# Kernel tuning notes

Hardware: AMD Instinct MI355X
Metric: run time of the kernel (lower is better)

## Reference

```python
import jax, jax.numpy as jnp
import numpy as np

BS, SL, FD = 8192, 49, 11
D_MODEL, DM2, HEAD = 128, 64, 8
NH, NHID, NLAYER = DM2 // HEAD, 4, 2
ABF = 1.0
XY_IDX = np.array([0, 1, 2, 3, 4, 5, 6, 7, 10])  # x feats + y feat (batch-normed cols)
DEC_IN = D_MODEL + 10  # d_model + len(x_dims + spa_dims)


def tanhshrink(x):
    return x - jnp.tanh(x)


def rope_angles(spa):
    # spa: [bs, sl, 2] -> per-token block angles [bs, sl, 4]
    # block order matches torch.block_diag(Rx(t0), Ry(t0), Rx(t1), Ry(t1))
    thetas = 10000.0 ** ((2.0 - 2.0 * jnp.arange(2, dtype=spa.dtype)) / 8.0)  # d=8, n_thetas=2
    ax = spa[..., 0:1] * thetas  # [bs, sl, 2]
    ay = spa[..., 1:2] * thetas
    return jnp.stack([ax[..., 0], ay[..., 0], ax[..., 1], ay[..., 1]], axis=-1)


def apply_rope(v, ang):
    # v: [bs, nh, s, 8]; ang: [bs, s, 4]. Applies the 8x8 block-diagonal
    # rotation directly on 2-d sub-pairs (same math as R @ v, no 8x8 matmats).
    c = jnp.cos(ang)[:, None]  # [bs, 1, s, 4]
    s = jnp.sin(ang)[:, None]
    v2 = v.reshape(*v.shape[:-1], 4, 2)
    r = jnp.stack([c * v2[..., 0] - s * v2[..., 1],
                   s * v2[..., 0] + c * v2[..., 1]], axis=-1)
    return r.reshape(v.shape)


def heads(x):  # [bs, s, dm2] -> [bs, nh, s, hd]
    b, s, _ = x.shape
    return x.reshape(b, s, NH, HEAD).transpose(0, 2, 1, 3)


def merge(x):  # [bs, nh, s, hd] -> [bs, s, dm2]
    b, h, s, d = x.shape
    return x.transpose(0, 2, 1, 3).reshape(b, s, h * d)


def mlp2(x, w1, b1, w2, b2):
    return tanhshrink(x @ w1 + b1) @ w2 + b2


def forward_impl(input_tensor, dists, bn_gamma, bn_beta,
                 xe_w1, xe_b1, xe_w2, xe_b2, ye_w1, ye_b1, ye_w2, ye_b2,
                 learnable_y, hidden_tokens, Wq, Wk, Wv, Wo, Wq2, Wk2, Wv2, Wo2,
                 dec_w0, dec_b0, dec_w1, dec_b1, dec_w2, dec_b2):
    bs = input_tensor.shape[0]
    # --- NanBatchNorm over x+y feature columns (no NaNs in clean inputs) ---
    xy = input_tensor[:, :, XY_IDX]
    mu = jnp.mean(xy, axis=(0, 1), keepdims=True)
    var = jnp.var(xy, axis=(0, 1), keepdims=True)
    xy = (xy - mu) / jnp.sqrt(var + 1e-5) * bn_gamma + bn_beta
    input_tensor = input_tensor.at[:, :, XY_IDX].set(xy)

    # --- target at last seq position: drop its dist, keep context dists ---
    dists_ctx = dists[:, :-1]                       # [bs, sl-1]
    central_x = input_tensor[:, -1:, :-1]           # [bs, 1, 10] (x + spa feats)

    # --- 2D RoPE angles from spatial coords ---
    ang = rope_angles(input_tensor[:, :, 8:10])     # [bs, sl, 4]

    # --- FCN encoders (two streams a=x, b=y) ---
    x_embed = mlp2(input_tensor[:, :, :8], xe_w1, xe_b1, xe_w2, xe_b2)      # [bs, sl, 64]
    y_embed = mlp2(input_tensor[:, :-1, 10:11], ye_w1, ye_b1, ye_w2, ye_b2)  # [bs, sl-1, 64]
    y_embed = jnp.concatenate([y_embed, jnp.broadcast_to(learnable_y, (bs, 1, DM2))], axis=1)

    ctx = (x_embed[:, :-1], y_embed[:, :-1])
    qry = (x_embed[:, -1:], y_embed[:, -1:])
    ang_ctx, ang_q = ang[:, :-1], ang[:, -1:]
    bias = (-ABF * dists_ctx)[:, None, None, :]     # [bs, 1, 1, sl-1]
    scale = 1.0 / jnp.sqrt(jnp.asarray(HEAD, input_tensor.dtype))

    outs, attn_ws = [], []
    for s in range(2):
        H = jnp.broadcast_to(hidden_tokens, (bs, NHID, DM2))
        for l in range(NLAYER):
            q = heads(H @ Wq[l, s])
            k = apply_rope(heads(ctx[s] @ Wk[l, s]), ang_ctx)
            v = heads(ctx[s] @ Wv[l, s])
            sc = jnp.einsum('bhqd,bhkd->bhqk', q, k) * scale + bias
            a = jax.nn.softmax(sc, axis=-1)
            H = H + merge(jnp.einsum('bhqk,bhkd->bhqd', a, v)) @ Wo[l, s]
        # query cross-attends the inducing tokens
        q = apply_rope(heads(qry[s] @ Wq2[s]), ang_q)
        k = heads(H @ Wk2[s])
        v = heads(H @ Wv2[s])
        sc = jnp.einsum('bhqd,bhkd->bhqk', q, k) * scale
        a = jax.nn.softmax(sc, axis=-1)
        outs.append(merge(jnp.einsum('bhqk,bhkd->bhqd', a, v)) @ Wo2[s])  # [bs, 1, 64]
        attn_ws.append(a)

    encoding = jnp.concatenate(outs, axis=-1)               # [bs, 1, 128]
    encoding = jnp.concatenate([encoding, central_x], axis=-1)  # [bs, 1, 138]
    h = tanhshrink(encoding @ dec_w0 + dec_b0)
    h = tanhshrink(h @ dec_w1 + dec_b1)
    pred = h @ dec_w2 + dec_b2                              # [bs, 1, 1]
    return pred


def setup_inputs() -> dict:
    key = jax.random.key(0)
    ks = jax.random.split(key, 32)
    g = lambda i, shape: 0.05 * jax.random.normal(ks[i], shape, dtype=jnp.float32)
    inp = {
        'input_tensor': jax.random.normal(ks[0], (BS, SL, FD), dtype=jnp.float32),
        'dists': jax.random.uniform(ks[1], (BS, SL), dtype=jnp.float32),
        'target_position': jnp.zeros((3, BS), dtype=jnp.int32),
        'bn_gamma': jnp.ones((9,), jnp.float32),
        'bn_beta': jnp.zeros((9,), jnp.float32),
        'xe_w1': g(2, (8, DM2)), 'xe_b1': jnp.zeros((DM2,), jnp.float32),
        'xe_w2': g(3, (DM2, DM2)), 'xe_b2': jnp.zeros((DM2,), jnp.float32),
        'ye_w1': g(4, (1, DM2)), 'ye_b1': jnp.zeros((DM2,), jnp.float32),
        'ye_w2': g(5, (DM2, DM2)), 'ye_b2': jnp.zeros((DM2,), jnp.float32),
        'learnable_y': g(6, (1, 1, DM2)),
        'hidden_tokens': g(7, (NHID, DM2)),
        'Wq': g(8, (NLAYER, 2, DM2, DM2)), 'Wk': g(9, (NLAYER, 2, DM2, DM2)),
        'Wv': g(10, (NLAYER, 2, DM2, DM2)), 'Wo': g(11, (NLAYER, 2, DM2, DM2)),
        'Wq2': g(12, (2, DM2, DM2)), 'Wk2': g(13, (2, DM2, DM2)),
        'Wv2': g(14, (2, DM2, DM2)), 'Wo2': g(15, (2, DM2, DM2)),
        'dec_w0': g(16, (DEC_IN, 512)), 'dec_b0': jnp.zeros((512,), jnp.float32),
        'dec_w1': g(17, (512, 256)), 'dec_b1': jnp.zeros((256,), jnp.float32),
        'dec_w2': g(18, (256, 1)), 'dec_b2': jnp.zeros((1,), jnp.float32),
    }
    return inp


def reference(input_tensor, dists, target_position, bn_gamma, bn_beta,
              xe_w1, xe_b1, xe_w2, xe_b2, ye_w1, ye_b1, ye_w2, ye_b2,
              learnable_y, hidden_tokens, Wq, Wk, Wv, Wo, Wq2, Wk2, Wv2, Wo2,
              dec_w0, dec_b0, dec_w1, dec_b1, dec_w2, dec_b2):
    # target_position is an index constant (query is the last token by construction)
    return forward_impl(input_tensor, dists, bn_gamma, bn_beta,
                        xe_w1, xe_b1, xe_w2, xe_b2, ye_w1, ye_b1, ye_w2, ye_b2,
                        learnable_y, hidden_tokens, Wq, Wk, Wv, Wo, Wq2, Wk2, Wv2, Wo2,
                        dec_w0, dec_b0, dec_w1, dec_b1, dec_w2, dec_b2)
```

## Files before the change

### kernel.cpp

```cpp
#include <hip/hip_runtime.h>
#include <math.h>

#define BS 8192
#define SL 49
#define FDIM 11
#define ROWS (BS*SL)

__device__ __forceinline__ float tanhshrink_f(float x) {
  float e = __expf(2.f * x);
  return (x - 1.f) + __fdividef(2.f, e + 1.f);
}

__global__ __launch_bounds__(256) void k_stats(const float* __restrict__ inp,
                                               double* __restrict__ gsum) {
  const int nblk = gridDim.x;
  const int per = (ROWS + nblk - 1) / nblk;
  const int r0 = blockIdx.x * per;
  int r1 = r0 + per; if (r1 > ROWS) r1 = ROWS;
  float s[9], q[9];
#pragma unroll
  for (int j = 0; j < 9; ++j) { s[j] = 0.f; q[j] = 0.f; }
  for (int r = r0 + threadIdx.x; r < r1; r += 256) {
    const float* row = inp + r * FDIM;
#pragma unroll
    for (int j = 0; j < 9; ++j) {
      float v = row[j < 8 ? j : 10];
      s[j] += v; q[j] += v * v;
    }
  }
#pragma unroll
  for (int j = 0; j < 9; ++j) {
    for (int off = 32; off; off >>= 1) {
      s[j] += __shfl_down(s[j], off);
      q[j] += __shfl_down(q[j], off);
    }
  }
  __shared__ float red[4][18];
  const int wid = threadIdx.x >> 6;
  const int lane = threadIdx.x & 63;
  if (lane == 0) {
#pragma unroll
    for (int j = 0; j < 9; ++j) { red[wid][j] = s[j]; red[wid][9 + j] = q[j]; }
  }
  __syncthreads();
  if (threadIdx.x < 18) {
    float t = red[0][threadIdx.x] + red[1][threadIdx.x] +
              red[2][threadIdx.x] + red[3][threadIdx.x];
    atomicAdd(&gsum[threadIdx.x], (double)t);
  }
}

__global__ __launch_bounds__(256) void k_pack(const float* __restrict__ xe_w1,
                          const float* __restrict__ xe_w2,
                          const float* __restrict__ ye_w2,
                          const float* __restrict__ Wk,
                          const float* __restrict__ Wq,
                          const float* __restrict__ Wv,
                          const float* __restrict__ Wo,
                          const float* __restrict__ Wq2,
                          const float* __restrict__ Wk2,
                          const float* __restrict__ Wv2,
                          const float* __restrict__ Wo2,
                          float* __restrict__ xw1T,
                          float* __restrict__ we2,
                          float* __restrict__ wk4,
                          float* __restrict__ wpk) {
  int gid = blockIdx.x * 256 + threadIdx.x;
  if (gid < 512) { int cc = gid >> 3, k = gid & 7; xw1T[gid] = xe_w1[k * 64 + cc]; }
  {
    int i = gid;
    int ss = i >> 12, r = i & 4095, kc = r >> 8, cc = (r >> 2) & 63, kk = r & 3;
    const float* W2 = ss ? ye_w2 : xe_w2;
    we2[i] = W2[(4 * kc + kk) * 64 + cc];
  }
  for (int i = gid; i < 16384; i += 8192) {
    int ls = i >> 12, r = i & 4095, kc = r >> 8, cc = (r >> 2) & 63, kk = r & 3;
    wk4[i] = Wk[ls * 4096 + (4 * kc + kk) * 64 + cc];
  }
  for (int i = gid; i < 18 * 4096; i += 8192) {
    int m = i >> 12, r = i & 4095, c4 = r >> 8, lane = (r >> 2) & 63, j = r & 3;
    const float* src;
    if      (m < 4)  src = Wv  + (m << 12);
    else if (m < 8)  src = Wo  + ((m - 4) << 12);
    else if (m < 10) src = Wq  + ((2 + (m - 8)) << 12);
    else if (m < 12) src = Wq2 + ((m - 10) << 12);
    else if (m < 14) src = Wk2 + ((m - 12) << 12);
    else if (m < 16) src = Wv2 + ((m - 14) << 12);
    else             src = Wo2 + ((m - 16) << 12);
    wpk[i] = src[(4 * c4 + j) * 64 + lane];
  }
}

__global__ __launch_bounds__(256) void k_finalize(const double* __restrict__ gsum,
                           const float* __restrict__ gamma,
                           const float* __restrict__ beta,
                           const float* __restrict__ hidden,
                           const float* __restrict__ Wq,
                           float* __restrict__ bnp,
                           float* __restrict__ q0g) {
  int tid = threadIdx.x;
  if (tid < 9) {
    const double N = (double)ROWS;
    double mean = gsum[tid] / N;
    double msq  = gsum[9 + tid] / N;
    float var = (float)(msq - mean * mean);
    float sc = gamma[tid] / sqrtf(var + 1e-5f);
    bnp[tid] = sc;
    bnp[9 + tid] = beta[tid] - (float)mean * sc;
  }
  int s = tid >> 7, i2 = (tid >> 6) & 1, c = tid & 63;
  const float* W = Wq + (s << 12);
#pragma unroll
  for (int ii = 0; ii < 2; ++ii) {
    int i = i2 + 2 * ii;
    float a = 0.f;
    for (int k = 0; k < 64; ++k) a += hidden[i * 64 + k] * W[k * 64 + c];
    q0g[s * 256 + i * 64 + c] = a;
  }
}

__global__ __launch_bounds__(256, 4) void k_mega(
    const float* __restrict__ inp, const float* __restrict__ dists,
    const float* __restrict__ bnp, const float* __restrict__ q0g,
    const float* __restrict__ xw1T, const float* __restrict__ xe_b1,
    const float* __restrict__ we2, const float* __restrict__ xe_b2,
    const float* __restrict__ ye_w1, const float* __restrict__ ye_b1,
    const float* __restrict__ ye_b2,
    const float* __restrict__ learnable_y, const float* __restrict__ hidden_tokens,
    const float* __restrict__ wk4, const float* __restrict__ wpk,
    float* __restrict__ enc)
{
  __shared__ float raw[49][12];
  __shared__ float cs8T[8][52];
  __shared__ float embs[49 * 68];
  __shared__ float KB[49][68];
  __shared__ float scb[32][52];
  __shared__ float Hs[4][64];
  __shared__ float qb[4][64];
  __shared__ float db[48];
  __shared__ float bnl[18];
  __shared__ float q2[64];
  __shared__ float o1[64];
  __shared__ float a2[32];

  const int tid  = threadIdx.x;
  const int lane = tid & 63;
  const int grp  = tid >> 6;
  const int wg   = __builtin_amdgcn_readfirstlane(grp);
  const int b    = blockIdx.x >> 1;
  const int s    = blockIdx.x & 1;
  const float scale = 0.35355339059327373f;

  for (int i = tid; i < 49 * FDIM; i += 256) raw[i / FDIM][i % FDIM] = inp[b * (49*FDIM) + i];
  if (tid < 18) bnl[tid] = bnp[tid];
  if (tid >= 64 && tid < 112) db[tid - 64] = dists[b * 49 + (tid - 64)];
  __syncthreads();

  if (tid < 49) {
    float x = raw[tid][8], y = raw[tid][9];
    cs8T[0][tid] = cosf(10.f * x); cs8T[1][tid] = cosf(10.f * y);
    cs8T[2][tid] = cosf(x);        cs8T[3][tid] = cosf(y);
    cs8T[4][tid] = sinf(10.f * x); cs8T[5][tid] = sinf(10.f * y);
    cs8T[6][tid] = sinf(x);        cs8T[7][tid] = sinf(y);
  }
  for (int i = tid; i < 441; i += 256) {
    int t = i / 9, j = i - t * 9;
    int f = (j < 8) ? j : 10;
    raw[t][f] = raw[t][f] * bnl[j] + bnl[9 + j];
  }
  __syncthreads();

  if (s == 0 && tid < 10) enc[b * 138 + 128 + tid] = raw[48][tid];

  if (s == 0) {
    if (lane < 49) {
      float4 r0 = *(const float4*)&raw[lane][0];
      float4 r1 = *(const float4*)&raw[lane][4];
      const float* w = xw1T + wg * 128;
      float h[16];
#pragma unroll
      for (int ci = 0; ci < 16; ++ci) {
        float a = xe_b1[wg * 16 + ci]
                + r0.x * w[ci*8+0] + r0.y * w[ci*8+1] + r0.z * w[ci*8+2] + r0.w * w[ci*8+3]
                + r1.x * w[ci*8+4] + r1.y * w[ci*8+5] + r1.z * w[ci*8+6] + r1.w * w[ci*8+7];
        h[ci] = tanhshrink_f(a);
      }
#pragma unroll
      for (int i = 0; i < 4; ++i)
        *(float4*)&KB[lane][wg * 16 + 4 * i] = make_float4(h[4*i], h[4*i+1], h[4*i+2], h[4*i+3]);
    }
  } else {
    if (lane < 48) {
      float ry = raw[lane][10];
      float h[16];
#pragma unroll
      for (int ci = 0; ci < 16; ++ci)
        h[ci] = tanhshrink_f(ry * ye_w1[wg * 16 + ci] + ye_b1[wg * 16 + ci]);
#pragma unroll
      for (int i = 0; i < 4; ++i)
        *(float4*)&KB[lane][wg * 16 + 4 * i] = make_float4(h[4*i], h[4*i+1], h[4*i+2], h[4*i+3]);
    }
  }
  __syncthreads();

  {
    const int nrow = (s == 0) ? 49 : 48;
    const float* WE = we2 + (s << 12);
    const float* bb = (s == 0) ? xe_b2 : ye_b2;
    if (lane < nrow) {
      float o[16];
#pragma unroll
      for (int ci = 0; ci < 16; ++ci) o[ci] = bb[wg * 16 + ci];
      for (int kc = 0; kc < 16; ++kc) {
        float4 e = *(const float4*)&KB[lane][kc * 4];
        const float* w = WE + (kc << 8) + (wg << 6);
#pragma unroll
        for (int ci = 0; ci < 16; ++ci)
          o[ci] += e.x * w[ci*4+0] + e.y * w[ci*4+1] + e.z * w[ci*4+2] + e.w * w[ci*4+3];
      }
#pragma unroll
      for (int i = 0; i < 4; ++i)
        *(float4*)&embs[lane * 68 + wg * 16 + 4 * i] = make_float4(o[4*i], o[4*i+1], o[4*i+2], o[4*i+3]);
    }
    if (s == 1 && tid < 64) embs[48 * 68 + lane] = learnable_y[lane];
  }
  Hs[grp][lane] = hidden_tokens[grp * 64 + lane];
  __syncthreads();

#pragma unroll 1
  for (int l = 0; l < 2; ++l) {
    if (l == 0) {
      qb[grp][lane] = q0g[s * 256 + tid];
    } else {
      const float* WqP = wpk + ((8 + s) << 12);
      float a = 0.f;
      for (int k4 = 0; k4 < 16; ++k4) {
        float4 hv = *(const float4*)&Hs[grp][k4 * 4];
        float4 w  = *(const float4*)&WqP[(k4 << 8) + (lane << 2)];
        a += hv.x * w.x + hv.y * w.y + hv.z * w.z + hv.w * w.w;
      }
      qb[grp][lane] = a;
    }
    if (lane < 48) {
      float o[16];
#pragma unroll
      for (int ci = 0; ci < 16; ++ci) o[ci] = 0.f;
      const float* WK = wk4 + ((l * 2 + s) << 12);
      for (int kc = 0; kc < 16; ++kc) {
        float4 e = *(const float4*)&embs[lane * 68 + kc * 4];
        const float* w = WK + (kc << 8) + (wg << 6);
#pragma unroll
        for (int ci = 0; ci < 16; ++ci)
          o[ci] += e.x * w[ci*4+0] + e.y * w[ci*4+1] + e.z * w[ci*4+2] + e.w * w[ci*4+3];
      }
      float ko[16];
#pragma unroll
      for (int i = 0; i < 8; ++i) {
        int p = i & 3;
        float co = cs8T[p][lane], si = cs8T[4 + p][lane];
        ko[2*i]   = co * o[2*i] - si * o[2*i+1];
        ko[2*i+1] = si * o[2*i] + co * o[2*i+1];
      }
#pragma unroll
      for (int i = 0; i < 4; ++i)
        *(float4*)&KB[lane][wg * 16 + 4 * i] = make_float4(ko[4*i], ko[4*i+1], ko[4*i+2], ko[4*i+3]);
    }
    __syncthreads();
    {
      const int t0 = tid & 7;
      const int i  = (tid >> 3) & 3;
      const int h  = tid >> 5;
      const int r  = tid >> 3;
      float4 qa = *(const float4*)&qb[i][h * 8];
      float4 qc = *(const float4*)&qb[i][h * 8 + 4];
      float v[6];
#pragma unroll
      for (int j = 0; j < 6; ++j) {
        int t = t0 + 8 * j;
        float4 ka = *(const float4*)&KB[t][h * 8];
        float4 kc = *(const float4*)&KB[t][h * 8 + 4];
        float a = qa.x * ka.x + qa.y * ka.y + qa.z * ka.z + qa.w * ka.w
                + qc.x * kc.x + qc.y * kc.y + qc.z * kc.z + qc.w * kc.w;
        v[j] = a * scale - db[t];
      }
      float m = fmaxf(fmaxf(fmaxf(v[0], v[1]), fmaxf(v[2], v[3])), fmaxf(v[4], v[5]));
      m = fmaxf(m, __shfl_xor(m, 1));
      m = fmaxf(m, __shfl_xor(m, 2));
      m = fmaxf(m, __shfl_xor(m, 4));
      float sum = 0.f;
#pragma unroll
      for (int j = 0; j < 6; ++j) { v[j] = __expf(v[j] - m); sum += v[j]; }
      sum += __shfl_xor(sum, 1);
      sum += __shfl_xor(sum, 2);
      sum += __shfl_xor(sum, 4);
      float inv = 1.f / sum;
#pragma unroll
      for (int j = 0; j < 6; ++j) scb[r][t0 + 8 * j] = v[j] * inv;
    }
    __syncthreads();
    {
      float acc[8];
#pragma unroll
      for (int m = 0; m < 8; ++m) acc[m] = 0.f;
      for (int tt = 0; tt < 48; tt += 4) {
        float e0 = embs[(tt + 0) * 68 + lane], e1 = embs[(tt + 1) * 68 + lane];
        float e2 = embs[(tt + 2) * 68 + lane], e3 = embs[(tt + 3) * 68 + lane];
#pragma unroll
        for (int m = 0; m < 8; ++m) {
          float4 sc4 = *(const float4*)&scb[grp + 4 * m][tt];
          acc[m] += sc4.x * e0 + sc4.y * e1 + sc4.z * e2 + sc4.w * e3;
        }
      }
#pragma unroll
      for (int m = 0; m < 8; ++m) KB[grp + 4 * m][lane] = acc[m];
    }
    {
      const float* WvP = wpk + ((l * 2 + s) << 12);
      const int r = ((lane >> 3) << 2) + grp;
      float a = 0.f;
      for (int c4 = 0; c4 < 16; ++c4) {
        float4 tv = *(const float4*)&KB[r][c4 * 4];
        float4 w  = *(const float4*)&WvP[(c4 << 8) + (lane << 2)];
        a += tv.x * w.x + tv.y * w.y + tv.z * w.z + tv.w * w.w;
      }
      qb[grp][lane] = a;
    }
    {
      const float* WoP = wpk + ((4 + l * 2 + s) << 12);
      float a = Hs[grp][lane];
      for (int k4 = 0; k4 < 16; ++k4) {
        float4 av = *(const float4*)&qb[grp][k4 * 4];
        float4 w  = *(const float4*)&WoP[(k4 << 8) + (lane << 2)];
        a += av.x * w.x + av.y * w.y + av.z * w.z + av.w * w.w;
      }
      Hs[grp][lane] = a;
    }
    if (l == 0) __syncthreads();
  }

  if (tid < 64) {
    const float* WqP = wpk + ((10 + s) << 12);
    float a = 0.f;
    for (int k4 = 0; k4 < 16; ++k4) {
      float4 cv = *(const float4*)&embs[48 * 68 + k4 * 4];
      float4 w  = *(const float4*)&WqP[(k4 << 8) + (lane << 2)];
      a += cv.x * w.x + cv.y * w.y + cv.z * w.z + cv.w * w.w;
    }
    float other = __shfl_xor(a, 1);
    int p = (lane >> 1) & 3;
    float co = cs8T[p][48], si = cs8T[4 + p][48];
    q2[lane] = (lane & 1) ? (si * other + co * a) : (co * a - si * other);
  }
  {
    const float* WkP = wpk + ((12 + s) << 12);
    const float* WvP = wpk + ((14 + s) << 12);
    float aK = 0.f, aV = 0.f;
    for (int k4 = 0; k4 < 16; ++k4) {
      float4 hv = *(const float4*)&Hs[grp][k4 * 4];
      float4 wk = *(const float4*)&WkP[(k4 << 8) + (lane << 2)];
      float4 wv = *(const float4*)&WvP[(k4 << 8) + (lane << 2)];
      aK += hv.x * wk.x + hv.y * wk.y + hv.z * wk.z + hv.w * wk.w;
      aV += hv.x * wv.x + hv.y * wv.y + hv.z * wv.z + hv.w * wv.w;
    }
    KB[grp][lane] = aK;
    KB[8 + grp][lane] = aV;
  }
  __syncthreads();
  if (tid < 32) {
    int h = tid >> 2, i = tid & 3;
    float a = 0.f;
#pragma unroll
    for (int d = 0; d < 8; ++d) a += q2[h * 8 + d] * KB[i][h * 8 + d];
    a *= scale;
    float m = fmaxf(a, __shfl_xor(a, 1));
    m = fmaxf(m, __shfl_xor(m, 2));
    float e = __expf(a - m);
    float sum = e + __shfl_xor(e, 1);
    sum += __shfl_xor(sum, 2);
    a2[tid] = e / sum;
  }
  if (tid < 64) {
    int h = lane >> 3;
    float a = 0.f;
#pragma unroll
    for (int i = 0; i < 4; ++i) a += a2[h * 4 + i] * KB[8 + i][lane];
    o1[lane] = a;
  }
  if (tid < 64) {
    const float* WoP = wpk + ((16 + s) << 12);
    float a = 0.f;
    for (int k4 = 0; k4 < 16; ++k4) {
      float4 ov = *(const float4*)&o1[k4 * 4];
      float4 w  = *(const float4*)&WoP[(k4 << 8) + (lane << 2)];
      a += ov.x * w.x + ov.y * w.y + ov.z * w.z + ov.w * w.w;
    }
    enc[b * 138 + s * 64 + lane] = a;
  }
}

__global__ __launch_bounds__(256, 5) void k_dec(
    const float* __restrict__ enc,
    const float* __restrict__ w0, const float* __restrict__ b0,
    const float* __restrict__ w1, const float* __restrict__ b1,
    const float* __restrict__ w2, const float* __restrict__ b2,
    float* __restrict__ out)
{
  __shared__ float encs[8][140];
  __shared__ float h0s[8][512];
  __shared__ float h1s[8][256];
  const int tid = threadIdx.x;
  const int rb = blockIdx.x * 8;

  for (int i = tid; i < 8 * 138; i += 256) {
    int r = i / 138, k = i - r * 138;
    encs[r][k] = enc[(rb + r) * 138 + k];
  }
  __syncthreads();
  {
    float acc0[8], acc1[8];
    const float bb0 = b0[tid], bb1 = b0[tid + 256];
#pragma unroll
    for (int r = 0; r < 8; ++r) { acc0[r] = bb0; acc1[r] = bb1; }
    for (int k = 0; k < 136; k += 4) {
      float wa0 = w0[(k + 0) * 512 + tid], wa1 = w0[(k + 1) * 512 + tid];
      float wa2 = w0[(k + 2) * 512 + tid], wa3 = w0[(k + 3) * 512 + tid];
      float wb0 = w0[(k + 0) * 512 + tid + 256], wb1 = w0[(k + 1) * 512 + tid + 256];
      float wb2 = w0[(k + 2) * 512 + tid + 256], wb3 = w0[(k + 3) * 512 + tid + 256];
#pragma unroll
      for (int r = 0; r < 8; ++r) {
        float4 ev = *(const float4*)&encs[r][k];
        acc0[r] += ev.x * wa0 + ev.y * wa1 + ev.z * wa2 + ev.w * wa3;
        acc1[r] += ev.x * wb0 + ev.y * wb1 + ev.z * wb2 + ev.w * wb3;
      }
    }
    for (int k = 136; k < 138; ++k) {
      float wa = w0[k * 512 + tid], wb = w0[k * 512 + tid + 256];
#pragma unroll
      for (int r = 0; r < 8; ++r) {
        float e = encs[r][k];
        acc0[r] += e * wa; acc1[r] += e * wb;
      }
    }
#pragma unroll
    for (int r = 0; r < 8; ++r) {
      h0s[r][tid] = tanhshrink_f(acc0[r]);
      h0s[r][tid + 256] = tanhshrink_f(acc1[r]);
    }
  }
  __syncthreads();
  {
    float acc[8];
    const float bb = b1[tid];
#pragma unroll
    for (int r = 0; r < 8; ++r) acc[r] = bb;
    for (int k = 0; k < 512; k += 4) {
      float ww0 = w1[(k + 0) * 256 + tid], ww1 = w1[(k + 1) * 256 + tid];
      float ww2 = w1[(k + 2) * 256 + tid], ww3 = w1[(k + 3) * 256 + tid];
#pragma unroll
      for (int r = 0; r < 8; ++r) {
        float4 hv = *(const float4*)&h0s[r][k];
        acc[r] += hv.x * ww0 + hv.y * ww1 + hv.z * ww2 + hv.w * ww3;
      }
    }
#pragma unroll
    for (int r = 0; r < 8; ++r) h1s[r][tid] = tanhshrink_f(acc[r]);
  }
  __syncthreads();
  {
    int r = tid >> 5, l32 = tid & 31;
    float a = 0.f;
#pragma unroll
    for (int kk = 0; kk < 8; ++kk) {
      int k = l32 + 32 * kk;
      a += h1s[r][k] * w2[k];
    }
    for (int off = 16; off; off >>= 1) a += __shfl_down(a, off, 32);
    if (l32 == 0) out[rb + r] = a + b2[0];
  }
}

extern "C" void kernel_launch(void* const* d_in, const int* in_sizes, int n_in,
                              void* d_out, int out_size, void* d_ws, size_t ws_size,
                              hipStream_t stream) {
  const float* inp        = (const float*)d_in[0];
  const float* dists      = (const float*)d_in[1];
  const float* bn_gamma   = (const float*)d_in[3];
  const float* bn_beta    = (const float*)d_in[4];
  const float* xe_w1      = (const float*)d_in[5];
  const float* xe_b1      = (const float*)d_in[6];
  const float* xe_w2      = (const float*)d_in[7];
  const float* xe_b2      = (const float*)d_in[8];
  const float* ye_w1      = (const float*)d_in[9];
  const float* ye_b1      = (const float*)d_in[10];
  const float* ye_w2      = (const float*)d_in[11];
  const float* ye_b2      = (const float*)d_in[12];
  const float* learnable  = (const float*)d_in[13];
  const float* hidden     = (const float*)d_in[14];
  const float* Wq         = (const float*)d_in[15];
  const float* Wk         = (const float*)d_in[16];
  const float* Wv         = (const float*)d_in[17];
  const float* Wo         = (const float*)d_in[18];
  const float* Wq2        = (const float*)d_in[19];
  const float* Wk2        = (const float*)d_in[20];
  const float* Wv2        = (const float*)d_in[21];
  const float* Wo2        = (const float*)d_in[22];
  const float* dec_w0     = (const float*)d_in[23];
  const float* dec_b0     = (const float*)d_in[24];
  const float* dec_w1     = (const float*)d_in[25];
  const float* dec_b1     = (const float*)d_in[26];
  const float* dec_w2     = (const float*)d_in[27];
  const float* dec_b2     = (const float*)d_in[28];

  double* gsum = (double*)d_ws;
  float*  bnp  = (float*)((char*)d_ws + 256);
  float*  q0g  = (float*)((char*)d_ws + 512);
  float*  enc  = (float*)((char*)d_ws + 2560);
  float*  xw1T = (float*)((char*)d_ws + 4524544);
  float*  we2  = (float*)((char*)d_ws + 4526592);
  float*  wk4  = (float*)((char*)d_ws + 4559360);
  float*  wpk  = (float*)((char*)d_ws + 4624896);

  hipMemsetAsync(d_ws, 0, 256, stream);
  k_pack    <<<32, 256, 0, stream>>>(xe_w1, xe_w2, ye_w2, Wk, Wq, Wv, Wo,
                                     Wq2, Wk2, Wv2, Wo2, xw1T, we2, wk4, wpk);
  k_stats   <<<512, 256, 0, stream>>>(inp, gsum);
  k_finalize<<<1, 256, 0, stream>>>(gsum, bn_gamma, bn_beta, hidden, Wq, bnp, q0g);
  k_mega    <<<BS * 2, 256, 0, stream>>>(inp, dists, bnp, q0g,
                                         xw1T, xe_b1, we2, xe_b2,
                                         ye_w1, ye_b1, ye_b2,
                                         learnable, hidden,
                                         wk4, wpk, enc);
  k_dec     <<<BS / 8, 256, 0, stream>>>(enc, dec_w0, dec_b0, dec_w1, dec_b1,
                                         dec_w2, dec_b2, (float*)d_out);
}
```

Measured before the change: 938.5 us.

## Widen k_mega blocks to 512 threads, halving per-thread column work

Result: slower. 1.451 ms (+54.6%).

```diff
diff --git a/kernel.cpp b/kernel.cpp
--- a/kernel.cpp
+++ b/kernel.cpp
@@ -119,7 +119,7 @@
   }
 }
 
-__global__ __launch_bounds__(256, 4) void k_mega(
+__global__ __launch_bounds__(512, 8) void k_mega(
     const float* __restrict__ inp, const float* __restrict__ dists,
     const float* __restrict__ bnp, const float* __restrict__ q0g,
     const float* __restrict__ xw1T, const float* __restrict__ xe_b1,
@@ -134,7 +134,7 @@
   __shared__ float cs8T[8][52];
   __shared__ float embs[49 * 68];
   __shared__ float KB[49][68];
-  __shared__ float scb[32][52];
+  __shared__ float scb[32][48];
   __shared__ float Hs[4][64];
   __shared__ float qb[4][64];
   __shared__ float db[48];
@@ -151,7 +151,7 @@
   const int s    = blockIdx.x & 1;
   const float scale = 0.35355339059327373f;
 
-  for (int i = tid; i < 49 * FDIM; i += 256) raw[i / FDIM][i % FDIM] = inp[b * (49*FDIM) + i];
+  for (int i = tid; i < 49 * FDIM; i += 512) raw[i / FDIM][i % FDIM] = inp[b * (49*FDIM) + i];
   if (tid < 18) bnl[tid] = bnp[tid];
   if (tid >= 64 && tid < 112) db[tid - 64] = dists[b * 49 + (tid - 64)];
   __syncthreads();
@@ -163,7 +163,7 @@
     cs8T[4][tid] = sinf(10.f * x); cs8T[5][tid] = sinf(10.f * y);
     cs8T[6][tid] = sinf(x);        cs8T[7][tid] = sinf(y);
   }
-  for (int i = tid; i < 441; i += 256) {
+  for (int i = tid; i < 441; i += 512) {
     int t = i / 9, j = i - t * 9;
     int f = (j < 8) ? j : 10;
     raw[t][f] = raw[t][f] * bnl[j] + bnl[9 + j];
@@ -176,29 +176,27 @@
     if (lane < 49) {
       float4 r0 = *(const float4*)&raw[lane][0];
       float4 r1 = *(const float4*)&raw[lane][4];
-      const float* w = xw1T + wg * 128;
-      float h[16];
-#pragma unroll
-      for (int ci = 0; ci < 16; ++ci) {
-        float a = xe_b1[wg * 16 + ci]
+      const float* w = xw1T + wg * 64;
+      float h[8];
+#pragma unroll
+      for (int ci = 0; ci < 8; ++ci) {
+        float a = xe_b1[wg * 8 + ci]
                 + r0.x * w[ci*8+0] + r0.y * w[ci*8+1] + r0.z * w[ci*8+2] + r0.w * w[ci*8+3]
                 + r1.x * w[ci*8+4] + r1.y * w[ci*8+5] + r1.z * w[ci*8+6] + r1.w * w[ci*8+7];
         h[ci] = tanhshrink_f(a);
       }
-#pragma unroll
-      for (int i = 0; i < 4; ++i)
-        *(float4*)&KB[lane][wg * 16 + 4 * i] = make_float4(h[4*i], h[4*i+1], h[4*i+2], h[4*i+3]);
+      *(float4*)&KB[lane][wg * 8 + 0] = make_float4(h[0], h[1], h[2], h[3]);
+      *(float4*)&KB[lane][wg * 8 + 4] = make_float4(h[4], h[5], h[6], h[7]);
     }
   } else {
     if (lane < 48) {
       float ry = raw[lane][10];
-      float h[16];
-#pragma unroll
-      for (int ci = 0; ci < 16; ++ci)
-        h[ci] = tanhshrink_f(ry * ye_w1[wg * 16 + ci] + ye_b1[wg * 16 + ci]);
-#pragma unroll
-      for (int i = 0; i < 4; ++i)
-        *(float4*)&KB[lane][wg * 16 + 4 * i] = make_float4(h[4*i], h[4*i+1], h[4*i+2], h[4*i+3]);
+      float h[8];
+#pragma unroll
+      for (int ci = 0; ci < 8; ++ci)
+        h[ci] = tanhshrink_f(ry * ye_w1[wg * 8 + ci] + ye_b1[wg * 8 + ci]);
+      *(float4*)&KB[lane][wg * 8 + 0] = make_float4(h[0], h[1], h[2], h[3]);
+      *(float4*)&KB[lane][wg * 8 + 4] = make_float4(h[4], h[5], h[6], h[7]);
     }
   }
   __syncthreads();
@@ -208,124 +206,132 @@
     const float* WE = we2 + (s << 12);
     const float* bb = (s == 0) ? xe_b2 : ye_b2;
     if (lane < nrow) {
-      float o[16];
-#pragma unroll
-      for (int ci = 0; ci < 16; ++ci) o[ci] = bb[wg * 16 + ci];
+      float o[8];
+#pragma unroll
+      for (int ci = 0; ci < 8; ++ci) o[ci] = bb[wg * 8 + ci];
       for (int kc = 0; kc < 16; ++kc) {
         float4 e = *(const float4*)&KB[lane][kc * 4];
-        const float* w = WE + (kc << 8) + (wg << 6);
-#pragma unroll
-        for (int ci = 0; ci < 16; ++ci)
+        const float* w = WE + (kc << 8) + (wg << 5);
+#pragma unroll
+        for (int ci = 0; ci < 8; ++ci)
           o[ci] += e.x * w[ci*4+0] + e.y * w[ci*4+1] + e.z * w[ci*4+2] + e.w * w[ci*4+3];
       }
-#pragma unroll
-      for (int i = 0; i < 4; ++i)
-        *(float4*)&embs[lane * 68 + wg * 16 + 4 * i] = make_float4(o[4*i], o[4*i+1], o[4*i+2], o[4*i+3]);
+      *(float4*)&embs[lane * 68 + wg * 8 + 0] = make_float4(o[0], o[1], o[2], o[3]);
+      *(float4*)&embs[lane * 68 + wg * 8 + 4] = make_float4(o[4], o[5], o[6], o[7]);
     }
     if (s == 1 && tid < 64) embs[48 * 68 + lane] = learnable_y[lane];
   }
-  Hs[grp][lane] = hidden_tokens[grp * 64 + lane];
+  if (tid < 256) Hs[grp][lane] = hidden_tokens[grp * 64 + lane];
   __syncthreads();
 
 #pragma unroll 1
   for (int l = 0; l < 2; ++l) {
     if (l == 0) {
-      qb[grp][lane] = q0g[s * 256 + tid];
+      if (tid < 256) qb[grp][lane] = q0g[s * 256 + tid];
     } else {
-      const float* WqP = wpk + ((8 + s) << 12);
-      float a = 0.f;
-      for (int k4 = 0; k4 < 16; ++k4) {
-        float4 hv = *(const float4*)&Hs[grp][k4 * 4];
-        float4 w  = *(const float4*)&WqP[(k4 << 8) + (lane << 2)];
-        a += hv.x * w.x + hv.y * w.y + hv.z * w.z + hv.w * w.w;
-      }
-      qb[grp][lane] = a;
+      if (tid < 256) {
+        const float* WqP = wpk + ((8 + s) << 12);
+        float a = 0.f;
+        for (int k4 = 0; k4 < 16; ++k4) {
+          float4 hv = *(const float4*)&Hs[grp][k4 * 4];
+          float4 w  = *(const float4*)&WqP[(k4 << 8) + (lane << 2)];
+          a += hv.x * w.x + hv.y * w.y + hv.z * w.z + hv.w * w.w;
+        }
+        qb[grp][lane] = a;
+      }
     }
     if (lane < 48) {
-      float o[16];
-#pragma unroll
-      for (int ci = 0; ci < 16; ++ci) o[ci] = 0.f;
+      float o[8];
+#pragma unroll
+      for (int ci = 0; ci < 8; ++ci) o[ci] = 0.f;
       const float* WK = wk4 + ((l * 2 + s) << 12);
       for (int kc = 0; kc < 16; ++kc) {
         float4 e = *(const float4*)&embs[lane * 68 + kc * 4];
-        const float* w = WK + (kc << 8) + (wg << 6);
-#pragma unroll
-        for (int ci = 0; ci < 16; ++ci)
+        const float* w = WK + (kc << 8) + (wg << 5);
+#pragma unroll
+        for (int ci = 0; ci < 8; ++ci)
           o[ci] += e.x * w[ci*4+0] + e.y * w[ci*4+1] + e.z * w[ci*4+2] + e.w * w[ci*4+3];
       }
-      float ko[16];
-#pragma unroll
-      for (int i = 0; i < 8; ++i) {
+      float ko[8];
+#pragma unroll
+      for (int i = 0; i < 4; ++i) {
         int p = i & 3;
         float co = cs8T[p][lane], si = cs8T[4 + p][lane];
         ko[2*i]   = co * o[2*i] - si * o[2*i+1];
         ko[2*i+1] = si * o[2*i] + co * o[2*i+1];
       }
-#pragma unroll
-      for (int i = 0; i < 4; ++i)
-        *(float4*)&KB[lane][wg * 16 + 4 * i] = make_float4(ko[4*i], ko[4*i+1], ko[4*i+2], ko[4*i+3]);
+      *(float4*)&KB[lane][wg * 8 + 0] = make_float4(ko[0], ko[1], ko[2], ko[3]);
+      *(float4*)&KB[lane][wg * 8 + 4] = make_float4(ko[4], ko[5], ko[6], ko[7]);
     }
     __syncthreads();
     {
-      const int t0 = tid & 7;
-      const int i  = (tid >> 3) & 3;
-      const int h  = tid >> 5;
-      const int r  = tid >> 3;
+      const int r   = tid >> 4;
+      const int t16 = tid & 15;
+      const int i   = r & 3;
+      const int h   = r >> 2;
       float4 qa = *(const float4*)&qb[i][h * 8];
       float4 qc = *(const float4*)&qb[i][h * 8 + 4];
-      float v[6];
-#pragma unroll
-      for (int j = 0; j < 6; ++j) {
-        int t = t0 + 8 * j;
+      float v[3];
+#pragma unroll
+      for (int j = 0; j < 3; ++j) {
+        int t = t16 + 16 * j;
         float4 ka = *(const float4*)&KB[t][h * 8];
         float4 kc = *(const float4*)&KB[t][h * 8 + 4];
         float a = qa.x * ka.x + qa.y * ka.y + qa.z * ka.z + qa.w * ka.w
                 + qc.x * kc.x + qc.y * kc.y + qc.z * kc.z + qc.w * kc.w;
         v[j] = a * scale - db[t];
       }
-      float m = fmaxf(fmaxf(fmaxf(v[0], v[1]), fmaxf(v[2], v[3])), fmaxf(v[4], v[5]));
+      float m = fmaxf(fmaxf(v[0], v[1]), v[2]);
       m = fmaxf(m, __shfl_xor(m, 1));
       m = fmaxf(m, __shfl_xor(m, 2));
       m = fmaxf(m, __shfl_xor(m, 4));
+      m = fmaxf(m, __shfl_xor(m, 8));
       float sum = 0.f;
 #pragma unroll
-      for (int j = 0; j < 6; ++j) { v[j] = __expf(v[j] - m); sum += v[j]; }
+      for (int j = 0; j < 3; ++j) { v[j] = __expf(v[j] - m); sum += v[j]; }
       sum += __shfl_xor(sum, 1);
       sum += __shfl_xor(sum, 2);
       sum += __shfl_xor(sum, 4);
+      sum += __shfl_xor(sum, 8);
       float inv = 1.f / sum;
 #pragma unroll
-      for (int j = 0; j < 6; ++j) scb[r][t0 + 8 * j] = v[j] * inv;
+      for (int j = 0; j < 3; ++j) scb[r][t16 + 16 * j] = v[j] * inv;
     }
     __syncthreads();
     {
-      float acc[8];
-#pragma unroll
-      for (int m = 0; m < 8; ++m) acc[m] = 0.f;
+      float acc[4];
+#pragma unroll
+      for (int m = 0; m < 4; ++m) acc[m] = 0.f;
       for (int tt = 0; tt < 48; tt += 4) {
         float e0 = embs[(tt + 0) * 68 + lane], e1 = embs[(tt + 1) * 68 + lane];
         float e2 = embs[(tt + 2) * 68 + lane], e3 = embs[(tt + 3) * 68 + lane];
 #pragma unroll
-        for (int m = 0; m < 8; ++m) {
-          float4 sc4 = *(const float4*)&scb[grp + 4 * m][tt];
+        for (int m = 0; m < 4; ++m) {
+          float4 sc4 = *(const float4*)&scb[grp + 8 * m][tt];
           acc[m] += sc4.x * e0 + sc4.y * e1 + sc4.z * e2 + sc4.w * e3;
         }
       }
 #pragma unroll
-      for (int m = 0; m < 8; ++m) KB[grp + 4 * m][lane] = acc[m];
+      for (int m = 0; m < 4; ++m) KB[grp + 8 * m][lane] = acc[m];
     }
     {
-      const float* WvP = wpk + ((l * 2 + s) << 12);
-      const int r = ((lane >> 3) << 2) + grp;
-      float a = 0.f;
-      for (int c4 = 0; c4 < 16; ++c4) {
-        float4 tv = *(const float4*)&KB[r][c4 * 4];
-        float4 w  = *(const float4*)&WvP[(c4 << 8) + (lane << 2)];
-        a += tv.x * w.x + tv.y * w.y + tv.z * w.z + tv.w * w.w;
-      }
-      qb[grp][lane] = a;
-    }
-    {
+      const int hp = grp >> 2;
+      const int i  = grp & 3;
+      const int h  = lane >> 3;
+      if ((h & 1) == hp) {
+        const float* WvP = wpk + ((l * 2 + s) << 12);
+        const int r = h * 4 + i;
+        float a = 0.f;
+        for (int c4 = 0; c4 < 16; ++c4) {
+          float4 tv = *(const float4*)&KB[r][c4 * 4];
+          float4 w  = *(const float4*)&WvP[(c4 << 8) + (lane << 2)];
+          a += tv.x * w.x + tv.y * w.y + tv.z * w.z + tv.w * w.w;
+        }
+        qb[i][lane] = a;
+      }
+    }
+    __syncthreads();
+    if (tid < 256) {
       const float* WoP = wpk + ((4 + l * 2 + s) << 12);
       float a = Hs[grp][lane];
       for (int k4 = 0; k4 < 16; ++k4) {
@@ -335,7 +341,7 @@
       }
       Hs[grp][lane] = a;
     }
-    if (l == 0) __syncthreads();
+    __syncthreads();
   }
 
   if (tid < 64) {
@@ -351,7 +357,7 @@
     float co = cs8T[p][48], si = cs8T[4 + p][48];
     q2[lane] = (lane & 1) ? (si * other + co * a) : (co * a - si * other);
   }
-  {
+  if (tid < 256) {
     const float* WkP = wpk + ((12 + s) << 12);
     const float* WvP = wpk + ((14 + s) << 12);
     float aK = 0.f, aV = 0.f;
@@ -525,7 +531,7 @@
                                      Wq2, Wk2, Wv2, Wo2, xw1T, we2, wk4, wpk);
   k_stats   <<<512, 256, 0, stream>>>(inp, gsum);
   k_finalize<<<1, 256, 0, stream>>>(gsum, bn_gamma, bn_beta, hidden, Wq, bnp, q0g);
-  k_mega    <<<BS * 2, 256, 0, stream>>>(inp, dists, bnp, q0g,
+  k_mega    <<<BS * 2, 512, 0, stream>>>(inp, dists, bnp, q0g,
                                          xw1T, xe_b1, we2, xe_b2,
                                          ye_w1, ye_b1, ye_b2,
                                          learnable, hidden,
```
